# Performance work log

Measured on AMD Instinct MI355X. Metric: run time of the kernel, lower is better.

Reference implementation:

```python
import jax, jax.numpy as jnp
import numpy as np

B = 2048        # graphs
MAX_LEN = 254   # nodes per graph (pad target)
DIM = 64
NF = 78         # num_features_xd
DEG = 8
N = B * MAX_LEN         # 520192 nodes
E = N * DEG             # 4161536 edges
BN_EPS = 1e-5
LN_EPS = 1e-5


def setup_inputs() -> dict:
    key = jax.random.key(0)
    ks = jax.random.split(key, 24)
    x = jax.random.normal(ks[0], (N, NF), jnp.float32)
    # intra-graph random edges: (src, dst) within the same graph
    g = jax.random.randint(ks[1], (E,), 0, B)
    src = g * MAX_LEN + jax.random.randint(ks[2], (E,), 0, MAX_LEN)
    dst = g * MAX_LEN + jax.random.randint(ks[3], (E,), 0, MAX_LEN)
    edge_index = jnp.stack([src, dst]).astype(jnp.int32)
    batch = (jnp.arange(N) // MAX_LEN).astype(jnp.int32)
    batch_len = jnp.full((B,), MAX_LEN, jnp.int32)

    def lin(k, fan_in, shape):
        return jax.random.uniform(k, shape, jnp.float32, -1.0, 1.0) / np.sqrt(fan_in)

    # conv1 MLP: 78->64->64
    w1a = lin(ks[4], NF, (NF, DIM)); b1a = lin(ks[5], NF, (DIM,))
    w1b = lin(ks[6], DIM, (DIM, DIM)); b1b = lin(ks[7], DIM, (DIM,))
    # convs 2-5 stacked: 64->64->64
    Wa = lin(ks[8], DIM, (4, DIM, DIM)); ba = lin(ks[9], DIM, (4, DIM))
    Wb = lin(ks[10], DIM, (4, DIM, DIM)); bb = lin(ks[11], DIM, (4, DIM))
    bn_gamma = jnp.ones((5, DIM), jnp.float32)
    bn_beta = jnp.zeros((5, DIM), jnp.float32)
    fc_w = lin(ks[12], DIM, (DIM, DIM)); fc_b = lin(ks[13], DIM, (DIM,))
    ln_gamma = jnp.ones((DIM,), jnp.float32)
    ln_beta = jnp.zeros((DIM,), jnp.float32)
    return {
        "x": x, "edge_index": edge_index, "batch": batch,
        "batch_len": batch_len, "max_len": MAX_LEN,
        "w1a": w1a, "b1a": b1a, "w1b": w1b, "b1b": b1b,
        "Wa": Wa, "ba": ba, "Wb": Wb, "bb": bb,
        "bn_gamma": bn_gamma, "bn_beta": bn_beta,
        "fc_w": fc_w, "fc_b": fc_b,
        "ln_gamma": ln_gamma, "ln_beta": ln_beta,
    }


def _gin_layer(h, src, dst, n, W1, b1, W2, b2, gamma, beta):
    # GINConv (eps=0): z_i = MLP(x_i + sum_{j->i} x_j), then ReLU, then BatchNorm (batch stats)
    agg = jax.ops.segment_sum(h[src], dst, num_segments=n)
    z = h + agg
    z = jnp.maximum(z @ W1 + b1, 0.0) @ W2 + b2
    z = jnp.maximum(z, 0.0)
    mean = z.mean(axis=0)
    var = jnp.square(z - mean).mean(axis=0)  # biased var, as torch BN training
    return (z - mean) * jax.lax.rsqrt(var + BN_EPS) * gamma + beta


def reference(x, edge_index, batch, batch_len, max_len,
              w1a, b1a, w1b, b1b, Wa, ba, Wb, bb,
              bn_gamma, bn_beta, fc_w, fc_b, ln_gamma, ln_beta):
    n = x.shape[0]
    src, dst = edge_index[0], edge_index[1]
    h = _gin_layer(x, src, dst, n, w1a, b1a, w1b, b1b, bn_gamma[0], bn_beta[0])
    for i in range(4):
        h = _gin_layer(h, src, dst, n, Wa[i], ba[i], Wb[i], bb[i],
                       bn_gamma[i + 1], bn_beta[i + 1])
    # get_nodes_att_f: pad per-graph node features to [B, max_len, dim]
    nb = batch_len.shape[0]
    offsets = jnp.cumsum(batch_len) - batch_len            # start index of each graph
    pos = jnp.arange(n, dtype=jnp.int32) - offsets[batch]  # node position within graph
    x_seq = jnp.zeros((nb, max_len, h.shape[1]), h.dtype).at[batch, pos].set(h)
    # global_add_pool + fc + relu + (dropout eval: identity) + layernorm
    pooled = jax.ops.segment_sum(h, batch, num_segments=nb)
    y = jnp.maximum(pooled @ fc_w + fc_b, 0.0)
    mu = y.mean(axis=-1, keepdims=True)
    var = jnp.square(y - mu).mean(axis=-1, keepdims=True)
    y = (y - mu) * jax.lax.rsqrt(var + LN_EPS) * ln_gamma + ln_beta
    return (x_seq, y)
```

## Files before the change

kernel.cpp:

```cpp
#include <hip/hip_runtime.h>

#define NGRAPH 2048
#define MAXLEN 254
#define NNODE 520192
#define NEDGE 4161536
#define NF 78
#define CAP 32
#define BN_EPS 1e-5f
#define LN_EPS 1e-5f

#define REP16A(F) F(0) F(1) F(2) F(3) F(4) F(5) F(6) F(7) \
                  F(8) F(9) F(10) F(11) F(12) F(13) F(14) F(15)
#define REP16B(F) F(0) F(1) F(2) F(3) F(4) F(5) F(6) F(7) \
                  F(8) F(9) F(10) F(11) F(12) F(13) F(14) F(15)

__global__ __launch_bounds__(256) void k_init(int* __restrict__ deg, float* __restrict__ stats) {
    int i = blockIdx.x * 256 + threadIdx.x;
    deg[i] = 0;
    if (blockIdx.x == 0) {
        for (int j = threadIdx.x; j < 5 * 128; j += 256) stats[j] = 0.f;
    }
}

__global__ __launch_bounds__(256) void k_build(const int* __restrict__ ei,
                                               int* __restrict__ deg,
                                               unsigned char* __restrict__ elist) {
    int e = blockIdx.x * 256 + threadIdx.x;
    int s = ei[e];
    int d = ei[NEDGE + e];
    int g = d / MAXLEN;
    int r = atomicAdd(&deg[d], 1);
    elist[(size_t)d * CAP + r] = (unsigned char)(s - g * MAXLEN);
}

__global__ __launch_bounds__(256) void k_gemm78(const float* __restrict__ x,
                                                const float* __restrict__ W,
                                                float* __restrict__ out) {
    __shared__ float sW[NF * 64];
    for (int i = threadIdx.x; i < NF * 64; i += 256) sW[i] = W[i];
    __syncthreads();
    int node = blockIdx.x * 256 + threadIdx.x;
    const float* xr = x + (size_t)node * NF;
    float a[64];
#pragma unroll
    for (int c = 0; c < 64; c++) a[c] = 0.f;
    for (int k2 = 0; k2 < NF / 2; k2++) {
        float2 xv = ((const float2*)xr)[k2];
        const float* w0 = sW + (2 * k2) * 64;
#pragma unroll
        for (int c = 0; c < 64; c++) a[c] += xv.x * w0[c];
#pragma unroll
        for (int c = 0; c < 64; c++) a[c] += xv.y * w0[64 + c];
    }
    float* orow = out + ((size_t)node << 6);
#pragma unroll
    for (int c = 0; c < 64; c += 4)
        *(float4*)(orow + c) = make_float4(a[c], a[c + 1], a[c + 2], a[c + 3]);
}

template <int FIRST>
__global__ __launch_bounds__(256, 2) void k_layer(const float* __restrict__ hin,
                                                  const unsigned char* __restrict__ elist,
                                                  const int* __restrict__ deg,
                                                  const float* __restrict__ stats,
                                                  const float* __restrict__ gamma,
                                                  const float* __restrict__ beta,
                                                  const float* __restrict__ W1,
                                                  const float* __restrict__ b1,
                                                  const float* __restrict__ W2,
                                                  const float* __restrict__ b2,
                                                  float* __restrict__ hout) {
    __shared__ float ssc[64], sbi[64];
    if constexpr (!FIRST) {
        if (threadIdx.x < 64) {
            int c = threadIdx.x;
            const float invN = 1.0f / NNODE;
            float mean = stats[c] * invN;
            float var = stats[64 + c] * invN - mean * mean;
            float sc = gamma[c] * rsqrtf(var + BN_EPS);
            ssc[c] = sc;
            sbi[c] = beta[c] - mean * sc;
        }
        __syncthreads();
    }

    int lb = (int)(blockIdx.x & 7) * 254 + (int)(blockIdx.x >> 3);
    int node = lb * 256 + threadIdx.x;
    int dg = deg[node];
    int base = (node / MAXLEN) * MAXLEN;

#define DECLG(i) float4 g##i;
    REP16A(DECLG)
    const float4* hr4 = (const float4*)(hin + ((size_t)node << 6));
#define LOADG(i) g##i = hr4[i];
    REP16A(LOADG)
    const unsigned* rowu = (const unsigned*)(elist + (size_t)node * CAP);
    int ne4 = (dg + 3) >> 2;
    unsigned pk = rowu[0];
    for (int e4 = 0; e4 < ne4; e4++) {
        unsigned nxt = rowu[e4 + 1];
#pragma unroll
        for (int j = 0; j < 4; j++) {
            if (4 * e4 + j < dg) {
                const float4* sr4 =
                    (const float4*)(hin + ((size_t)(base + (int)((pk >> (8 * j)) & 255u)) << 6));
#define ADDG(i) { float4 v_ = sr4[i]; g##i.x += v_.x; g##i.y += v_.y; \
                  g##i.z += v_.z; g##i.w += v_.w; }
                REP16A(ADDG)
            }
        }
        pk = nxt;
    }
    float kk = (float)(1 + dg);
    if constexpr (!FIRST) {
#define BNG(i) { const float4 s_ = *(const float4*)(ssc + 4 * (i)); \
                 const float4 b_ = *(const float4*)(sbi + 4 * (i)); \
                 g##i.x = g##i.x * s_.x + kk * b_.x; g##i.y = g##i.y * s_.y + kk * b_.y; \
                 g##i.z = g##i.z * s_.z + kk * b_.z; g##i.w = g##i.w * s_.w + kk * b_.w; }
        REP16A(BNG)
    }

#define DECLA(i) float4 a##i;
    REP16A(DECLA)
    const float4* b1q = (const float4*)b1;
    if constexpr (FIRST) {
#define AFROMG(i) { float4 b_ = b1q[i]; a##i.x = fmaxf(g##i.x + b_.x, 0.f); \
                    a##i.y = fmaxf(g##i.y + b_.y, 0.f); a##i.z = fmaxf(g##i.z + b_.z, 0.f); \
                    a##i.w = fmaxf(g##i.w + b_.w, 0.f); }
        REP16A(AFROMG)
    } else {
#define AINIT(i) a##i = b1q[i];
        REP16A(AINIT)
        const float4* W1q = (const float4*)W1;
#define AFMA(i) { float4 w_ = w4_[i]; a##i.x += ak_ * w_.x; a##i.y += ak_ * w_.y; \
                  a##i.z += ak_ * w_.z; a##i.w += ak_ * w_.w; }
#define MLP1K(K4) { const float4 r_ = g##K4; const float4* wb_ = W1q + (K4) * 64; \
    { const float ak_ = r_.x; const float4* w4_ = wb_;      REP16B(AFMA) } \
    { const float ak_ = r_.y; const float4* w4_ = wb_ + 16; REP16B(AFMA) } \
    { const float ak_ = r_.z; const float4* w4_ = wb_ + 32; REP16B(AFMA) } \
    { const float ak_ = r_.w; const float4* w4_ = wb_ + 48; REP16B(AFMA) } }
        REP16A(MLP1K)
#define RELUA(i) a##i.x = fmaxf(a##i.x, 0.f); a##i.y = fmaxf(a##i.y, 0.f); \
                 a##i.z = fmaxf(a##i.z, 0.f); a##i.w = fmaxf(a##i.w, 0.f);
        REP16A(RELUA)
    }

#define DECLO(i) float4 o##i;
    REP16A(DECLO)
    const float4* b2q = (const float4*)b2;
#define OINIT(i) o##i = b2q[i];
    REP16A(OINIT)
    const float4* W2q = (const float4*)W2;
#define OFMA(i) { float4 w_ = w4_[i]; o##i.x += ak_ * w_.x; o##i.y += ak_ * w_.y; \
                  o##i.z += ak_ * w_.z; o##i.w += ak_ * w_.w; }
#define MLP2K(K4) { const float4 r_ = a##K4; const float4* wb_ = W2q + (K4) * 64; \
    { const float ak_ = r_.x; const float4* w4_ = wb_;      REP16B(OFMA) } \
    { const float ak_ = r_.y; const float4* w4_ = wb_ + 16; REP16B(OFMA) } \
    { const float ak_ = r_.z; const float4* w4_ = wb_ + 32; REP16B(OFMA) } \
    { const float ak_ = r_.w; const float4* w4_ = wb_ + 48; REP16B(OFMA) } }
    REP16A(MLP2K)
    float4* out4 = (float4*)(hout + ((size_t)node << 6));
#define STOREO(i) out4[i] = make_float4(fmaxf(o##i.x, 0.f), fmaxf(o##i.y, 0.f), \
                                        fmaxf(o##i.z, 0.f), fmaxf(o##i.w, 0.f));
    REP16A(STOREO)
}

__global__ __launch_bounds__(256) void k_bnstats(const float* __restrict__ h,
                                                 float* __restrict__ stats) {
    __shared__ float ss[128];
    if (threadIdx.x < 128) ss[threadIdx.x] = 0.f;
    __syncthreads();
    int tid = blockIdx.x * 256 + threadIdx.x;
    int c4 = (tid & 15) * 4;
    float s0 = 0, s1 = 0, s2 = 0, s3 = 0, q0 = 0, q1 = 0, q2 = 0, q3 = 0;
    const float4* p = (const float4*)h;
    for (size_t i = tid; i < (size_t)NNODE * 16; i += 65536) {
        float4 v = p[i];
        s0 += v.x; q0 += v.x * v.x;
        s1 += v.y; q1 += v.y * v.y;
        s2 += v.z; q2 += v.z * v.z;
        s3 += v.w; q3 += v.w * v.w;
    }
    atomicAdd(&ss[c4], s0);      atomicAdd(&ss[c4 + 1], s1);
    atomicAdd(&ss[c4 + 2], s2);  atomicAdd(&ss[c4 + 3], s3);
    atomicAdd(&ss[64 + c4], q0); atomicAdd(&ss[64 + c4 + 1], q1);
    atomicAdd(&ss[64 + c4 + 2], q2); atomicAdd(&ss[64 + c4 + 3], q3);
    __syncthreads();
    if (threadIdx.x < 128) atomicAdd(&stats[threadIdx.x], ss[threadIdx.x]);
}

__global__ __launch_bounds__(256) void k_final(float* __restrict__ h,
                                               const float* __restrict__ stats,
                                               const float* __restrict__ gamma,
                                               const float* __restrict__ beta,
                                               const float* __restrict__ fcw,
                                               const float* __restrict__ fcb,
                                               const float* __restrict__ lng,
                                               const float* __restrict__ lnb,
                                               float* __restrict__ y) {
    int b = blockIdx.x;
    int q = threadIdx.x >> 6;
    int c = threadIdx.x & 63;
    __shared__ float ssc[64], sbi[64];
    if (threadIdx.x < 64) {
        const float invN = 1.0f / NNODE;
        float mean = stats[c] * invN;
        float var = stats[64 + c] * invN - mean * mean;
        float sc = gamma[c] * rsqrtf(var + BN_EPS);
        ssc[c] = sc;
        sbi[c] = beta[c] - mean * sc;
    }
    __syncthreads();
    float* base = h + (size_t)b * MAXLEN * 64;
    float sc = ssc[c], bi = sbi[c];
    float s = 0.f;
    for (int p = q; p < MAXLEN; p += 4) {
        float v = base[p * 64 + c] * sc + bi;
        base[p * 64 + c] = v;
        s += v;
    }
    __shared__ float sp[4][64];
    sp[q][c] = s;
    __syncthreads();
    __shared__ float pooled[64];
    if (threadIdx.x < 64) pooled[c] = sp[0][c] + sp[1][c] + sp[2][c] + sp[3][c];
    __syncthreads();
    if (threadIdx.x < 64) {
        float accv = fcb[c];
        for (int k = 0; k < 64; k++) accv += pooled[k] * fcw[k * 64 + c];
        accv = fmaxf(accv, 0.f);
        float t = accv;
        for (int o = 32; o; o >>= 1) t += __shfl_xor(t, o, 64);
        float mu = t * (1.0f / 64.0f);
        float d = accv - mu;
        float t2 = d * d;
        for (int o = 32; o; o >>= 1) t2 += __shfl_xor(t2, o, 64);
        float var = t2 * (1.0f / 64.0f);
        y[(size_t)b * 64 + c] = d * rsqrtf(var + LN_EPS) * lng[c] + lnb[c];
    }
}

extern "C" void kernel_launch(void* const* d_in, const int* in_sizes, int n_in,
                              void* d_out, int out_size, void* d_ws, size_t ws_size,
                              hipStream_t stream) {
    const float* x   = (const float*)d_in[0];
    const int*   ei  = (const int*)d_in[1];
    const float* w1a = (const float*)d_in[5];
    const float* b1a = (const float*)d_in[6];
    const float* w1b = (const float*)d_in[7];
    const float* b1b = (const float*)d_in[8];
    const float* Wa  = (const float*)d_in[9];
    const float* ba  = (const float*)d_in[10];
    const float* Wb  = (const float*)d_in[11];
    const float* bb  = (const float*)d_in[12];
    const float* bng = (const float*)d_in[13];
    const float* bnb = (const float*)d_in[14];
    const float* fcw = (const float*)d_in[15];
    const float* fcb = (const float*)d_in[16];
    const float* lng = (const float*)d_in[17];
    const float* lnb = (const float*)d_in[18];

    float* h   = (float*)d_out;
    float* y   = h + (size_t)NNODE * 64;
    float* acc = (float*)d_ws;
    float* stats = acc + (size_t)NNODE * 64;
    int* deg = (int*)(stats + 5 * 128);
    unsigned char* elist = (unsigned char*)(deg + NNODE);

    const int NB_NODE = NNODE / 256;
    const int NB_EDGE = NEDGE / 256;
    (void)in_sizes; (void)n_in; (void)out_size; (void)ws_size;

    k_init<<<NB_NODE, 256, 0, stream>>>(deg, stats);
    k_build<<<NB_EDGE, 256, 0, stream>>>(ei, deg, elist);

    k_gemm78<<<NB_NODE, 256, 0, stream>>>(x, w1a, acc);
    k_layer<1><<<NB_NODE, 256, 0, stream>>>(acc, elist, deg, nullptr, nullptr, nullptr,
                                            nullptr, b1a, w1b, b1b, h);
    k_bnstats<<<256, 256, 0, stream>>>(h, stats);

    for (int L = 1; L <= 4; L++) {
        const float* in = (L & 1) ? h : acc;
        float* out      = (L & 1) ? acc : h;
        k_layer<0><<<NB_NODE, 256, 0, stream>>>(in, elist, deg,
                                                stats + (size_t)(L - 1) * 128,
                                                bng + (size_t)(L - 1) * 64,
                                                bnb + (size_t)(L - 1) * 64,
                                                Wa + (size_t)(L - 1) * 4096,
                                                ba + (size_t)(L - 1) * 64,
                                                Wb + (size_t)(L - 1) * 4096,
                                                bb + (size_t)(L - 1) * 64, out);
        k_bnstats<<<256, 256, 0, stream>>>(out, stats + (size_t)L * 128);
    }

    k_final<<<NGRAPH, 256, 0, stream>>>(h, stats + 4 * 128, bng + 4 * 64, bnb + 4 * 64,
                                        fcw, fcb, lng, lnb, y);
}
```

Before: 2.638 ms.

## Stage MLP weights in LDS and fold BatchNorm affine into W1

Each block now copies W2 (and, for later layers, a BN-scaled W1) into shared memory, and precomputes a per-column bias term sbi·W1, so the per-node BN scale/shift is folded algebraically into the first matmul. The MLP inner loops read weights from LDS broadcasts instead of global/scalar loads. The aim is to remove per-node BN arithmetic and reduce weight-load latency. In exchange, every block pays setup cost and __syncthreads, and LDS use rises (~32KB), which may cap occupancy alongside the existing 2-blocks launch bound.

```diff
diff --git a/kernel.cpp b/kernel.cpp
--- a/kernel.cpp
+++ b/kernel.cpp
@@ -70,22 +70,37 @@
                                                   const float* __restrict__ W2,
                                                   const float* __restrict__ b2,
                                                   float* __restrict__ hout) {
+    __shared__ __align__(16) float sW1f[FIRST ? 4 : 64 * 64];
+    __shared__ __align__(16) float sW2[64 * 64];
+    __shared__ __align__(16) float sb1[64], sb2[64], ssu[64];
     __shared__ float ssc[64], sbi[64];
+    int tid = threadIdx.x;
+    if (tid < 64) {
+        sb1[tid] = b1[tid];
+        sb2[tid] = b2[tid];
+    }
     if constexpr (!FIRST) {
-        if (threadIdx.x < 64) {
-            int c = threadIdx.x;
+        if (tid < 64) {
             const float invN = 1.0f / NNODE;
-            float mean = stats[c] * invN;
-            float var = stats[64 + c] * invN - mean * mean;
-            float sc = gamma[c] * rsqrtf(var + BN_EPS);
-            ssc[c] = sc;
-            sbi[c] = beta[c] - mean * sc;
+            float mean = stats[tid] * invN;
+            float var = stats[64 + tid] * invN - mean * mean;
+            float sc = gamma[tid] * rsqrtf(var + BN_EPS);
+            ssc[tid] = sc;
+            sbi[tid] = beta[tid] - mean * sc;
         }
         __syncthreads();
-    }
+        for (int i = tid; i < 64 * 64; i += 256) sW1f[i] = ssc[i >> 6] * W1[i];
+        if (tid < 64) {
+            float s = 0.f;
+            for (int k = 0; k < 64; k++) s += sbi[k] * W1[k * 64 + tid];
+            ssu[tid] = s;
+        }
+    }
+    for (int i = tid; i < 64 * 64; i += 256) sW2[i] = W2[i];
+    __syncthreads();
 
     int lb = (int)(blockIdx.x & 7) * 254 + (int)(blockIdx.x >> 3);
-    int node = lb * 256 + threadIdx.x;
+    int node = lb * 256 + tid;
     int dg = deg[node];
     int base = (node / MAXLEN) * MAXLEN;
 
@@ -112,33 +127,28 @@
         pk = nxt;
     }
     float kk = (float)(1 + dg);
-    if constexpr (!FIRST) {
-#define BNG(i) { const float4 s_ = *(const float4*)(ssc + 4 * (i)); \
-                 const float4 b_ = *(const float4*)(sbi + 4 * (i)); \
-                 g##i.x = g##i.x * s_.x + kk * b_.x; g##i.y = g##i.y * s_.y + kk * b_.y; \
-                 g##i.z = g##i.z * s_.z + kk * b_.z; g##i.w = g##i.w * s_.w + kk * b_.w; }
-        REP16A(BNG)
-    }
+    (void)kk;
 
 #define DECLA(i) float4 a##i;
     REP16A(DECLA)
-    const float4* b1q = (const float4*)b1;
     if constexpr (FIRST) {
-#define AFROMG(i) { float4 b_ = b1q[i]; a##i.x = fmaxf(g##i.x + b_.x, 0.f); \
-                    a##i.y = fmaxf(g##i.y + b_.y, 0.f); a##i.z = fmaxf(g##i.z + b_.z, 0.f); \
-                    a##i.w = fmaxf(g##i.w + b_.w, 0.f); }
+#define AFROMG(i) { const float4 b_ = *(const float4*)(sb1 + 4 * (i)); \
+                    a##i.x = fmaxf(g##i.x + b_.x, 0.f); a##i.y = fmaxf(g##i.y + b_.y, 0.f); \
+                    a##i.z = fmaxf(g##i.z + b_.z, 0.f); a##i.w = fmaxf(g##i.w + b_.w, 0.f); }
         REP16A(AFROMG)
     } else {
-#define AINIT(i) a##i = b1q[i];
+#define AINIT(i) { const float4 b_ = *(const float4*)(sb1 + 4 * (i)); \
+                   const float4 u_ = *(const float4*)(ssu + 4 * (i)); \
+                   a##i.x = b_.x + kk * u_.x; a##i.y = b_.y + kk * u_.y; \
+                   a##i.z = b_.z + kk * u_.z; a##i.w = b_.w + kk * u_.w; }
         REP16A(AINIT)
-        const float4* W1q = (const float4*)W1;
 #define AFMA(i) { float4 w_ = w4_[i]; a##i.x += ak_ * w_.x; a##i.y += ak_ * w_.y; \
                   a##i.z += ak_ * w_.z; a##i.w += ak_ * w_.w; }
-#define MLP1K(K4) { const float4 r_ = g##K4; const float4* wb_ = W1q + (K4) * 64; \
-    { const float ak_ = r_.x; const float4* w4_ = wb_;      REP16B(AFMA) } \
-    { const float ak_ = r_.y; const float4* w4_ = wb_ + 16; REP16B(AFMA) } \
-    { const float ak_ = r_.z; const float4* w4_ = wb_ + 32; REP16B(AFMA) } \
-    { const float ak_ = r_.w; const float4* w4_ = wb_ + 48; REP16B(AFMA) } }
+#define MLP1K(K4) { const float4 r_ = g##K4; \
+    { const float ak_ = r_.x; const float4* w4_ = (const float4*)(sW1f + (4*(K4)+0)*64); REP16B(AFMA) } \
+    { const float ak_ = r_.y; const float4* w4_ = (const float4*)(sW1f + (4*(K4)+1)*64); REP16B(AFMA) } \
+    { const float ak_ = r_.z; const float4* w4_ = (const float4*)(sW1f + (4*(K4)+2)*64); REP16B(AFMA) } \
+    { const float ak_ = r_.w; const float4* w4_ = (const float4*)(sW1f + (4*(K4)+3)*64); REP16B(AFMA) } }
         REP16A(MLP1K)
 #define RELUA(i) a##i.x = fmaxf(a##i.x, 0.f); a##i.y = fmaxf(a##i.y, 0.f); \
                  a##i.z = fmaxf(a##i.z, 0.f); a##i.w = fmaxf(a##i.w, 0.f);
@@ -147,17 +157,15 @@
 
 #define DECLO(i) float4 o##i;
     REP16A(DECLO)
-    const float4* b2q = (const float4*)b2;
-#define OINIT(i) o##i = b2q[i];
+#define OINIT(i) o##i = *(const float4*)(sb2 + 4 * (i));
     REP16A(OINIT)
-    const float4* W2q = (const float4*)W2;
 #define OFMA(i) { float4 w_ = w4_[i]; o##i.x += ak_ * w_.x; o##i.y += ak_ * w_.y; \
                   o##i.z += ak_ * w_.z; o##i.w += ak_ * w_.w; }
-#define MLP2K(K4) { const float4 r_ = a##K4; const float4* wb_ = W2q + (K4) * 64; \
-    { const float ak_ = r_.x; const float4* w4_ = wb_;      REP16B(OFMA) } \
-    { const float ak_ = r_.y; const float4* w4_ = wb_ + 16; REP16B(OFMA) } \
-    { const float ak_ = r_.z; const float4* w4_ = wb_ + 32; REP16B(OFMA) } \
-    { const float ak_ = r_.w; const float4* w4_ = wb_ + 48; REP16B(OFMA) } }
+#define MLP2K(K4) { const float4 r_ = a##K4; \
+    { const float ak_ = r_.x; const float4* w4_ = (const float4*)(sW2 + (4*(K4)+0)*64); REP16B(OFMA) } \
+    { const float ak_ = r_.y; const float4* w4_ = (const float4*)(sW2 + (4*(K4)+1)*64); REP16B(OFMA) } \
+    { const float ak_ = r_.z; const float4* w4_ = (const float4*)(sW2 + (4*(K4)+2)*64); REP16B(OFMA) } \
+    { const float ak_ = r_.w; const float4* w4_ = (const float4*)(sW2 + (4*(K4)+3)*64); REP16B(OFMA) } }
     REP16A(MLP2K)
     float4* out4 = (float4*)(hout + ((size_t)node << 6));
 #define STOREO(i) out4[i] = make_float4(fmaxf(o##i.x, 0.f), fmaxf(o##i.y, 0.f), \
```

After: 2.542 ms. 1.04x faster.
